# Optimization experiments

Measured on AMD Instinct MI355X. Metric: run time of the kernel, lower is better.

## Reference

```python
import jax, jax.numpy as jnp
import numpy as np

B, N, H, DH, ORDER, DEG = 64, 256, 8, 64, 4, 16
D = H * DH
TOTAL = B * N
E = TOTAL * DEG


def setup_inputs() -> dict:
    key = jax.random.key(0)
    ks = jax.random.split(key, 16)
    output = jax.random.normal(ks[0], (N, B, D), dtype=jnp.float32)
    # attention weights: positive, row-normalized like softmax output
    attn = jax.nn.softmax(jax.random.normal(ks[1], (B, H, N, N), dtype=jnp.float32), axis=-1)
    out_each_head = jax.random.normal(ks[2], (B, N, H, DH), dtype=jnp.float32)
    # random graph edges, endpoints within the same graph (global node ids)
    g = jax.random.randint(ks[3], (E,), 0, B)
    s = g * N + jax.random.randint(ks[4], (E,), 0, N)
    d = g * N + jax.random.randint(ks[5], (E,), 0, N)
    edge_index = jnp.stack([s, d], axis=0).astype(jnp.int64)
    # full graphs, no padding: feature_indices[:,0]=graph id, [:,1]=node pos
    fi = jnp.stack([jnp.repeat(jnp.arange(B), N), jnp.tile(jnp.arange(N), B)], axis=1).astype(jnp.int64)
    batch = fi[:, 0]
    sc = 0.1
    params = dict(
        W_gcn=jax.random.normal(ks[6], (ORDER, ORDER)) * sc,
        b_gcn=jnp.zeros((ORDER,), jnp.float32),
        W_lin=jax.random.normal(ks[7], (ORDER, ORDER)) * sc,
        b_lin=jnp.zeros((ORDER,), jnp.float32),
        W_cheb=jax.random.normal(ks[8], (ORDER, DH, DH)) * sc,
        b_cheb=jnp.zeros((DH,), jnp.float32),
        W_cat=jax.random.normal(ks[9], (2 * D, D)) * sc,
        b_cat=jnp.zeros((D,), jnp.float32),
        gamma=jnp.ones((D,), jnp.float32),
        beta=jnp.zeros((D,), jnp.float32),
    )
    return dict(output=output, attn=attn, out_each_head=out_each_head,
                edge_index=edge_index, feature_indices=fi, batch=batch, **params)


def reference(output, attn, out_each_head, edge_index, feature_indices, batch,
              W_gcn, b_gcn, W_lin, b_lin, W_cheb, b_cheb, W_cat, b_cat, gamma, beta):
    Bn, Hn, Nn, _ = attn.shape
    C = W_gcn.shape[0]
    total = Bn * Nn
    NT = Hn * total

    # ---- get_filter_coefficients: GCN over fully-connected attention graphs ----
    # edge weights are detached in the original (edge_weight.detach())
    A = jax.lax.stop_gradient(attn).transpose(1, 0, 2, 3).reshape(Hn * Bn, Nn, Nn)
    A_hat = A + jnp.eye(Nn, dtype=A.dtype)  # add self loops (weight 1)
    deg = A_hat.sum(axis=1)                 # deg_j = sum_i A_hat[i,j]
    dinv = jnp.where(deg > 0, jax.lax.rsqrt(deg), 0.0)  # (HB, N)
    # x = ones, so x @ W_gcn is a constant row = column sums of W_gcn
    w_row = W_gcn.sum(axis=0)               # (C,)
    s = jnp.einsum('bi,bij->bj', dinv, A_hat) * dinv     # (HB, N)
    x_c = jnp.tanh(s[:, :, None] * w_row + b_gcn)        # (HB, N, C)
    gap = x_c.mean(axis=1)                  # global avg pool per graph (HB, C)
    coeff = gap @ W_lin + b_lin             # (HB, C) rows ordered (head, batch)

    # ---- dynamic Chebyshev filtering per head on the input graph ----
    offsets = (jnp.arange(Hn) * total).astype(edge_index.dtype)
    src = (edge_index[0][None, :] + offsets[:, None]).reshape(-1)
    dst = (edge_index[1][None, :] + offsets[:, None]).reshape(-1)
    deg_n = jax.ops.segment_sum(jnp.ones(src.shape[0], jnp.float32), dst, num_segments=NT)
    dinv_n = jnp.where(deg_n > 0, jax.lax.rsqrt(deg_n), 0.0)
    norm_e = -(dinv_n[src] * dinv_n[dst])   # scaled Laplacian L_hat = -D^-1/2 A D^-1/2

    def prop(x):  # L_hat @ x via gather/scatter
        return jax.ops.segment_sum(norm_e[:, None] * x[src], dst, num_segments=NT)

    # nodes ordered (head, batch, node)
    x0 = out_each_head.transpose(2, 0, 1, 3).reshape(NT, DH)
    batch_all = (batch[None, :] + (jnp.arange(Hn) * Bn)[:, None]).reshape(-1)  # graph id h*B+b
    c_node = coeff[batch_all]               # (NT, ORDER) per-node dynamic coefficients

    T_prev, T_cur = x0, prop(x0)
    acc = c_node[:, 0:1] * (T_prev @ W_cheb[0]) + c_node[:, 1:2] * (T_cur @ W_cheb[1])
    for k in range(2, C):
        T_next = 2.0 * prop(T_cur) - T_prev
        acc = acc + c_node[:, k:k + 1] * (T_next @ W_cheb[k])
        T_prev, T_cur = T_cur, T_next
    acc = acc + b_cheb                      # (NT, DH)

    # regroup heads: (H, B*N, DH) -> (B*N, H*DH), scatter back to (N, B, D)
    filtered = acc.reshape(Hn, total, DH).transpose(1, 0, 2).reshape(total, Hn * DH)
    out_filtered = jnp.zeros_like(output).at[feature_indices[:, 1], feature_indices[:, 0], :].set(filtered)

    # skip connection + linear_cat + final LayerNorm
    out_cat = jnp.concatenate([output, out_filtered], axis=-1)
    out = out_cat @ W_cat + b_cat
    mu = out.mean(axis=-1, keepdims=True)
    var = ((out - mu) ** 2).mean(axis=-1, keepdims=True)
    out = (out - mu) * jax.lax.rsqrt(var + 1e-5) * gamma + beta
    return out
```

## Files before the change

kernel.cpp:

```cpp
#include <hip/hip_runtime.h>
#include <stdint.h>

#define Bq      64
#define Nq      256
#define Hq      8
#define DHq     64
#define TOTALq  16384
#define NTq     131072
#define Dq      512

typedef __attribute__((ext_vector_type(8))) short short8;
typedef __attribute__((ext_vector_type(4))) float floatx4;

__device__ __forceinline__ unsigned short f2bf(float f) {
    union { float f; unsigned int u; } c; c.f = f;
    unsigned int u = c.u;
    return (unsigned short)((u + 0x7fffu + ((u >> 16) & 1u)) >> 16);
}
__device__ __forceinline__ float bf2f(unsigned short u) {
    union { unsigned int u; float f; } c; c.u = ((unsigned int)u) << 16;
    return c.f;
}


__global__ void count_deg_kernel(const int* __restrict__ dstp, int* __restrict__ cnt, int E) {
    int e = blockIdx.x * 256 + threadIdx.x;
    if (e < E) atomicAdd(&cnt[dstp[e]], 1);
}

__global__ void pscatter_kernel(const int* __restrict__ srcp, const int* __restrict__ dstp,
                                const int* __restrict__ cnt, float* __restrict__ Pf, int E) {
    int e = blockIdx.x * 256 + threadIdx.x;
    if (e >= E) return;
    int s = srcp[e], d = dstp[e];
    int cs = cnt[s], cd = cnt[d];
    float dvs = (cs > 0) ? rsqrtf((float)cs) : 0.0f;
    float dvd = (cd > 0) ? rsqrtf((float)cd) : 0.0f;
    int g = d >> 8;
    atomicAdd(&Pf[((size_t)g << 16) + ((size_t)(d & 255) << 8) + (s & 255)],
              -(dvs * dvd));
}

__global__ void pconv_kernel(const float* __restrict__ Pf, unsigned short* __restrict__ Pb) {
    int i = (blockIdx.x * 256 + threadIdx.x) * 4;
    float4 v = *(const float4*)(Pf + i);
    unsigned int lo = (unsigned int)f2bf(v.x) | ((unsigned int)f2bf(v.y) << 16);
    unsigned int hi = (unsigned int)f2bf(v.z) | ((unsigned int)f2bf(v.w) << 16);
    *(uint2*)(Pb + i) = make_uint2(lo, hi);
}

__global__ void prep_kernel(const float* __restrict__ Wcat, unsigned short* __restrict__ Wt2,
                            const float* __restrict__ Wch, float* __restrict__ WchTf) {
    int bid = blockIdx.x;
    if (bid < 256) {
        int idx = bid * 256 + threadIdx.x;
        int col = idx & 511;
        int ktq = idx >> 9;
        const float* src = Wcat + (size_t)(ktq * 8) * 512 + col;
        unsigned int pk[4];
#pragma unroll
        for (int q2 = 0; q2 < 4; ++q2) {
            unsigned short a = f2bf(src[(q2 * 2 + 0) * 512]);
            unsigned short b = f2bf(src[(q2 * 2 + 1) * 512]);
            pk[q2] = (unsigned int)a | ((unsigned int)b << 16);
        }
        *(uint4*)(Wt2 + (size_t)idx * 8) = make_uint4(pk[0], pk[1], pk[2], pk[3]);
    } else {
        int idx = (bid - 256) * 256 + threadIdx.x;
        int k = idx >> 12, rem = idx & 4095;
        int n = rem >> 6, j = rem & 63;
        WchTf[idx] = Wch[(k << 12) + (j << 6) + n];
    }
}

__global__ __launch_bounds__(512)
void coeff_kernel(const float* __restrict__ attn,
                  const float* __restrict__ Wg, const float* __restrict__ bg,
                  const float* __restrict__ Wlin, const float* __restrict__ blin,
                  float* __restrict__ coeff) {
    __shared__ floatx4 part[8][64];
    __shared__ floatx4 dinv4[64];
    const int g = blockIdx.x;
    const int h = g >> 6;
    const int b = g & 63;
    const float* A = attn + ((size_t)(b * Hq + h)) * (Nq * Nq);
    const int tid = threadIdx.x;
    const int rg = tid >> 6;
    const int cv = tid & 63;
    const float* Ap = A + cv * 4;

    floatx4 s1 = (floatx4){0.f, 0.f, 0.f, 0.f};
#pragma unroll 8
    for (int r = 0; r < 32; ++r)
        s1 += *(const floatx4*)(Ap + (size_t)(rg * 32 + r) * 256);
    part[rg][cv] = s1;
    __syncthreads();

    if (tid < 64) {
        floatx4 cs = part[0][tid];
#pragma unroll
        for (int i = 1; i < 8; ++i) cs += part[i][tid];
        floatx4 dv;
#pragma unroll
        for (int i = 0; i < 4; ++i) dv[i] = rsqrtf(cs[i] + 1.0f);
        dinv4[tid] = dv;
    }
    __syncthreads();

    const float* dsc = (const float*)dinv4;
    floatx4 s2 = (floatx4){0.f, 0.f, 0.f, 0.f};
#pragma unroll 8
    for (int r = 0; r < 32; ++r) {
        int rr = rg * 32 + r;
        s2 += dsc[rr] * (*(const floatx4*)(Ap + (size_t)rr * 256));
    }
    part[rg][cv] = s2;
    __syncthreads();

    if (tid < 64) {
        floatx4 ws = part[0][tid];
#pragma unroll
        for (int i = 1; i < 8; ++i) ws += part[i][tid];
        floatx4 dv = dinv4[tid];
        floatx4 sj = (ws + dv) * dv;

        float wr[4], bgl[4];
#pragma unroll
        for (int c = 0; c < 4; ++c) {
            wr[c]  = Wg[0 * 4 + c] + Wg[1 * 4 + c] + Wg[2 * 4 + c] + Wg[3 * 4 + c];
            bgl[c] = bg[c];
        }
        float v[4];
#pragma unroll
        for (int c = 0; c < 4; ++c) {
            v[c] = tanhf(sj[0] * wr[c] + bgl[c]) + tanhf(sj[1] * wr[c] + bgl[c]) +
                   tanhf(sj[2] * wr[c] + bgl[c]) + tanhf(sj[3] * wr[c] + bgl[c]);
#pragma unroll
            for (int o = 32; o >= 1; o >>= 1) v[c] += __shfl_down(v[c], o, 64);
        }
        float g0 = __shfl(v[0], 0, 64), g1 = __shfl(v[1], 0, 64);
        float g2 = __shfl(v[2], 0, 64), g3 = __shfl(v[3], 0, 64);
        if (tid < 4) {
            float r = blin[tid] + (g0 * Wlin[0 * 4 + tid] + g1 * Wlin[1 * 4 + tid] +
                                   g2 * Wlin[2 * 4 + tid] + g3 * Wlin[3 * 4 + tid]) *
                                      (1.0f / 256.0f);
            coeff[g * 4 + tid] = r;
        }
    }
}

__global__ __launch_bounds__(512, 2)
void cheb_fused(const unsigned short* __restrict__ Pb, const float* __restrict__ oeh,
                const float* __restrict__ WchTf, const float* __restrict__ coeff,
                const float* __restrict__ bch, unsigned short* __restrict__ filtb) {
    extern __shared__ unsigned char sm[];
    unsigned short* cm = (unsigned short*)sm;
    unsigned short* rm = (unsigned short*)(sm + 32768);
    unsigned short* Wl = (unsigned short*)(sm + 65536);

    const int g = blockIdx.x;
    const int b = (g & 7) * 8 + ((g >> 3) & 7);
    const int h = g >> 6;
    const int tid = threadIdx.x;
    const int lane = tid & 63, wv = tid >> 6;
    const int wr = wv >> 1, wc = wv & 1;
    const int quad = lane >> 4, l15 = lane & 15;

    const unsigned short* Pbase = Pb + ((size_t)b << 16);
    const float* cf = coeff + (h * 64 + b) * 4;

    {
        const int sn = tid >> 1;
        const int sh = (tid & 1) * 32;
        const float* sp = oeh + (size_t)(b * 256 + sn) * 512 + h * 64 + sh;
        unsigned int pk[16];
#pragma unroll
        for (int j = 0; j < 8; ++j) {
            float4 v = *(const float4*)(sp + j * 4);
            pk[2 * j]     = (unsigned)f2bf(v.x) | ((unsigned)f2bf(v.y) << 16);
            pk[2 * j + 1] = (unsigned)f2bf(v.z) | ((unsigned)f2bf(v.w) << 16);
        }
#pragma unroll
        for (int jj = 0; jj < 4; ++jj)
            *(uint4*)(rm + sn * 64 + ((((sh >> 3) + jj) ^ (sn & 7)) << 3)) =
                make_uint4(pk[4 * jj], pk[4 * jj + 1], pk[4 * jj + 2], pk[4 * jj + 3]);
#pragma unroll
        for (int e = 0; e < 32; ++e) {
            int c = sh + e;
            unsigned short v =
                (unsigned short)((e & 1) ? (pk[e >> 1] >> 16) : (pk[e >> 1] & 0xffffu));
            cm[c * 256 + (((sn >> 3) ^ (c & 31)) << 3) + (sn & 7)] = v;
        }
        float ck = cf[0];
        int r = tid >> 3, su = tid & 7;
        const float* wp = WchTf + r * 64 + su * 8;
        float4 w0 = *(const float4*)wp, w1 = *(const float4*)(wp + 4);
        *(uint4*)(Wl + r * 72 + su * 8) = make_uint4(
            (unsigned)f2bf(w0.x * ck) | ((unsigned)f2bf(w0.y * ck) << 16),
            (unsigned)f2bf(w0.z * ck) | ((unsigned)f2bf(w0.w * ck) << 16),
            (unsigned)f2bf(w1.x * ck) | ((unsigned)f2bf(w1.y * ck) << 16),
            (unsigned)f2bf(w1.z * ck) | ((unsigned)f2bf(w1.w * ck) << 16));
    }
    __syncthreads();

    unsigned int curp[4][2][2], prvp[4][2][2];
#pragma unroll
    for (int rt = 0; rt < 4; ++rt)
#pragma unroll
        for (int ct = 0; ct < 2; ++ct)
#pragma unroll
            for (int p = 0; p < 2; ++p) {
                int m = wr * 64 + rt * 16 + quad * 4 + 2 * p;
                int c = wc * 32 + ct * 16 + l15;
                curp[rt][ct][p] = *(const unsigned int*)(cm + c * 256 +
                                                         (((m >> 3) ^ (c & 31)) << 3) + (m & 7));
                prvp[rt][ct][p] = 0u;
            }

    floatx4 accf[4][2];
#pragma unroll
    for (int rt = 0; rt < 4; ++rt)
#pragma unroll
        for (int ct = 0; ct < 2; ++ct) accf[rt][ct] = (floatx4){0.f, 0.f, 0.f, 0.f};

#pragma unroll
    for (int k = 0; k < 4; ++k) {
#pragma unroll
        for (int kk = 0; kk < 2; ++kk) {
            short8 af[4], bfw[2];
#pragma unroll
            for (int rt = 0; rt < 4; ++rt) {
                int row = wr * 64 + rt * 16 + l15;
                af[rt] = *(const short8*)(rm + row * 64 + (((kk * 4 + quad) ^ (row & 7)) << 3));
            }
#pragma unroll
            for (int ct = 0; ct < 2; ++ct) {
                int oc = wc * 32 + ct * 16 + l15;
                bfw[ct] = *(const short8*)(Wl + oc * 72 + kk * 32 + quad * 8);
            }
#pragma unroll
            for (int rt = 0; rt < 4; ++rt)
#pragma unroll
                for (int ct = 0; ct < 2; ++ct)
                    accf[rt][ct] = __builtin_amdgcn_mfma_f32_16x16x32_bf16(
                        af[rt], bfw[ct], accf[rt][ct], 0, 0, 0);
        }
        if (k < 3) {
            floatx4 accp[4][2];
#pragma unroll
            for (int rt = 0; rt < 4; ++rt)
#pragma unroll
                for (int ct = 0; ct < 2; ++ct) accp[rt][ct] = (floatx4){0.f, 0.f, 0.f, 0.f};
#pragma unroll
            for (int kt = 0; kt < 8; ++kt) {
                short8 ap[4], bp[2];
#pragma unroll
                for (int rt = 0; rt < 4; ++rt) {
                    int row = wr * 64 + rt * 16 + l15;
                    ap[rt] = *(const short8*)(Pbase + row * 256 + kt * 32 + quad * 8);
                }
#pragma unroll
                for (int ct = 0; ct < 2; ++ct) {
                    int c = wc * 32 + ct * 16 + l15;
                    bp[ct] = *(const short8*)(cm + c * 256 + (((kt * 4 + quad) ^ (c & 31)) << 3));
                }
#pragma unroll
                for (int rt = 0; rt < 4; ++rt)
#pragma unroll
                    for (int ct = 0; ct < 2; ++ct)
                        accp[rt][ct] = __builtin_amdgcn_mfma_f32_16x16x32_bf16(
                            ap[rt], bp[ct], accp[rt][ct], 0, 0, 0);
            }
            __syncthreads();
#pragma unroll
            for (int rt = 0; rt < 4; ++rt)
#pragma unroll
                for (int ct = 0; ct < 2; ++ct)
#pragma unroll
                    for (int p = 0; p < 2; ++p) {
                        float a0 = accp[rt][ct][2 * p], a1 = accp[rt][ct][2 * p + 1];
                        if (k > 0) {
                            unsigned pv = prvp[rt][ct][p];
                            a0 = 2.0f * a0 - bf2f((unsigned short)(pv & 0xffffu));
                            a1 = 2.0f * a1 - bf2f((unsigned short)(pv >> 16));
                        }
                        unsigned nv = (unsigned)f2bf(a0) | ((unsigned)f2bf(a1) << 16);
                        prvp[rt][ct][p] = curp[rt][ct][p];
                        curp[rt][ct][p] = nv;
                        int m = wr * 64 + rt * 16 + quad * 4 + 2 * p;
                        int c = wc * 32 + ct * 16 + l15;
                        if (k < 2)
                            *(unsigned int*)(cm + c * 256 + (((m >> 3) ^ (c & 31)) << 3) +
                                             (m & 7)) = nv;
                        rm[m * 64 + (((c >> 3) ^ (m & 7)) << 3) + (c & 7)] =
                            (unsigned short)(nv & 0xffffu);
                        rm[(m + 1) * 64 + (((c >> 3) ^ ((m + 1) & 7)) << 3) + (c & 7)] =
                            (unsigned short)(nv >> 16);
                    }
            {
                float ck = cf[k + 1];
                int r = tid >> 3, su = tid & 7;
                const float* wp = WchTf + (k + 1) * 4096 + r * 64 + su * 8;
                float4 w0 = *(const float4*)wp, w1 = *(const float4*)(wp + 4);
                *(uint4*)(Wl + r * 72 + su * 8) = make_uint4(
                    (unsigned)f2bf(w0.x * ck) | ((unsigned)f2bf(w0.y * ck) << 16),
                    (unsigned)f2bf(w0.z * ck) | ((unsigned)f2bf(w0.w * ck) << 16),
                    (unsigned)f2bf(w1.x * ck) | ((unsigned)f2bf(w1.y * ck) << 16),
                    (unsigned)f2bf(w1.z * ck) | ((unsigned)f2bf(w1.w * ck) << 16));
            }
            __syncthreads();
        }
    }

    float bias[2];
#pragma unroll
    for (int ct = 0; ct < 2; ++ct) bias[ct] = bch[wc * 32 + ct * 16 + l15];
#pragma unroll
    for (int rt = 0; rt < 4; ++rt)
#pragma unroll
        for (int ct = 0; ct < 2; ++ct) {
            int c = wc * 32 + ct * 16 + l15;
#pragma unroll
            for (int i = 0; i < 4; ++i) {
                int m = wr * 64 + rt * 16 + quad * 4 + i;
                filtb[((size_t)m * 64 + b) * 512 + h * 64 + c] =
                    f2bf(accf[rt][ct][i] + bias[ct]);
            }
        }
}

__global__ __launch_bounds__(512, 2)
void gemm_ln_mfma(const float* __restrict__ outp, const unsigned short* __restrict__ filtb,
                  const unsigned short* __restrict__ Wt2, const float* __restrict__ bcat,
                  const float* __restrict__ gamma, const float* __restrict__ beta,
                  float* __restrict__ out) {
    extern __shared__ unsigned char smc[];
    unsigned short* A_lds0 = (unsigned short*)smc;
    unsigned short* A_lds1 = (unsigned short*)(smc + 4096);
    float* ep = (float*)smc;

    const int tid = threadIdx.x;
    const int lane = tid & 63;
    const int wv = tid >> 6;
    const int quad = lane >> 4;
    const int l15 = lane & 15;
    const int r0 = blockIdx.x * 64;

    const int s_row = tid >> 3;
    const int s_sub = tid & 7;
    const int s_q   = s_sub >> 1;
    const int s_e   = (s_sub & 1) * 4;

    const size_t boff = (size_t)(quad * 512 + wv * 64 + l15) * 8;

    floatx4 acc[4][4];
#pragma unroll
    for (int rt = 0; rt < 4; ++rt)
#pragma unroll
        for (int ct = 0; ct < 4; ++ct) acc[rt][ct] = (floatx4){0.f, 0.f, 0.f, 0.f};

    short8 bA[4], bB[4];
    float4 avX_f, avY_f;
    uint2  avX_b, avY_b;

    {
#pragma unroll
        for (int ct = 0; ct < 4; ++ct)
            bA[ct] = *(const short8*)(Wt2 + boff + ct * 128);
#pragma unroll
        for (int ct = 0; ct < 4; ++ct)
            bB[ct] = *(const short8*)(Wt2 + (size_t)16384 + boff + ct * 128);
        float4 av = *(const float4*)(outp + (size_t)(r0 + s_row) * 512 + s_sub * 4);
        avY_f = *(const float4*)(outp + (size_t)(r0 + s_row) * 512 + 32 + s_sub * 4);
        uint2 ap;
        ap.x = (unsigned int)f2bf(av.x) | ((unsigned int)f2bf(av.y) << 16);
        ap.y = (unsigned int)f2bf(av.z) | ((unsigned int)f2bf(av.w) << 16);
        *(uint2*)(A_lds0 + (s_q * 64 + s_row) * 8 + s_e) = ap;
        __syncthreads();
    }

#define GSTEP(KT, BCUR, AC, AN, AVCF, AVCB, AVNF, AVNB)                             \
    do {                                                                            \
        const int kt_ = (KT);                                                       \
        if (kt_ <= 29) {                                                            \
            const int kc2_ = (kt_ + 2) * 32;                                        \
            if (kc2_ < 512)                                                         \
                AVNF = *(const float4*)(outp + (size_t)(r0 + s_row) * 512 +         \
                                        kc2_ + s_sub * 4);                          \
            else                                                                    \
                AVNB = *(const uint2*)(filtb + (size_t)(r0 + s_row) * 512 +         \
                                       (kc2_ - 512) + s_sub * 4);                   \
        }                                                                           \
        short8 af_[4];                                                              \
        _Pragma("unroll")                                                           \
        for (int rt = 0; rt < 4; ++rt)                                              \
            af_[rt] = *(const short8*)(AC + (quad * 64 + rt * 16 + l15) * 8);       \
        _Pragma("unroll")                                                           \
        for (int rt = 0; rt < 4; ++rt)                                              \
            _Pragma("unroll")                                                       \
            for (int ct = 0; ct < 4; ++ct)                                          \
                acc[rt][ct] = __builtin_amdgcn_mfma_f32_16x16x32_bf16(              \
                    af_[rt], BCUR[ct], acc[rt][ct], 0, 0, 0);                       \
        if (kt_ <= 29) {                                                            \
            _Pragma("unroll")                                                       \
            for (int ct = 0; ct < 4; ++ct)                                          \
                BCUR[ct] = *(const short8*)(Wt2 + (size_t)(kt_ + 2) * 16384 +       \
                                            boff + ct * 128);                       \
        }                                                                           \
        if (kt_ <= 30) {                                                            \
            uint2 ap_;                                                              \
            if ((kt_ + 1) * 32 < 512) {                                             \
                ap_.x = (unsigned int)f2bf(AVCF.x) | ((unsigned int)f2bf(AVCF.y) << 16); \
                ap_.y = (unsigned int)f2bf(AVCF.z) | ((unsigned int)f2bf(AVCF.w) << 16); \
            } else {                                                                \
                ap_ = AVCB;                                                         \
            }                                                                       \
            *(uint2*)(AN + (s_q * 64 + s_row) * 8 + s_e) = ap_;                     \
        }                                                                           \
        asm volatile("s_waitcnt lgkmcnt(0)" ::: "memory");                          \
        __builtin_amdgcn_s_barrier();                                               \
        __builtin_amdgcn_sched_barrier(0);                                          \
    } while (0)

    for (int kt2 = 0; kt2 < 16; ++kt2) {
        GSTEP(2 * kt2,     bA, A_lds0, A_lds1, avY_f, avY_b, avX_f, avX_b);
        GSTEP(2 * kt2 + 1, bB, A_lds1, A_lds0, avX_f, avX_b, avY_f, avY_b);
    }
#undef GSTEP

    float gg[8], bb[8];
#pragma unroll
    for (int i = 0; i < 8; ++i) { gg[i] = gamma[i * 64 + lane]; bb[i] = beta[i * 64 + lane]; }
    float bc[4];
#pragma unroll
    for (int ct = 0; ct < 4; ++ct) bc[ct] = bcat[wv * 64 + ct * 16 + l15];

    for (int half = 0; half < 2; ++half) {
        __syncthreads();
#pragma unroll
        for (int rt2 = 0; rt2 < 2; ++rt2) {
            const int rt = half * 2 + rt2;
#pragma unroll
            for (int ct = 0; ct < 4; ++ct) {
                const int col = wv * 64 + ct * 16 + l15;
#pragma unroll
                for (int i = 0; i < 4; ++i) {
                    const int row_l = rt2 * 16 + quad * 4 + i;
                    ep[row_l * 512 + col] = acc[rt][ct][i] + bc[ct];
                }
            }
        }
        __syncthreads();
#pragma unroll
        for (int m4 = 0; m4 < 4; ++m4) {
            const int m = wv * 4 + m4;
            float s = 0.0f, ss = 0.0f;
#pragma unroll
            for (int i = 0; i < 8; ++i) {
                float v = ep[m * 512 + i * 64 + lane];
                s += v; ss += v * v;
            }
#pragma unroll
            for (int o = 32; o >= 1; o >>= 1) {
                s += __shfl_down(s, o, 64);
                ss += __shfl_down(ss, o, 64);
            }
            s = __shfl(s, 0, 64);
            ss = __shfl(ss, 0, 64);
            const float mu = s * (1.0f / 512.0f);
            const float var = ss * (1.0f / 512.0f) - mu * mu;
            const float rs = rsqrtf(var + 1e-5f);
            const int r = r0 + half * 32 + m;
#pragma unroll
            for (int i = 0; i < 8; ++i) {
                const int d = i * 64 + lane;
                out[(size_t)r * 512 + d] = (ep[m * 512 + d] - mu) * rs * gg[i] + bb[i];
            }
        }
    }
}

extern "C" void kernel_launch(void* const* d_in, const int* in_sizes, int n_in,
                              void* d_out, int out_size, void* d_ws, size_t ws_size,
                              hipStream_t stream) {
    const float* output       = (const float*)d_in[0];
    const float* attn         = (const float*)d_in[1];
    const float* oeh          = (const float*)d_in[2];
    const int*   edge_index   = (const int*)d_in[3];
    const float* W_gcn        = (const float*)d_in[6];
    const float* b_gcn        = (const float*)d_in[7];
    const float* W_lin        = (const float*)d_in[8];
    const float* b_lin        = (const float*)d_in[9];
    const float* W_cheb       = (const float*)d_in[10];
    const float* b_cheb       = (const float*)d_in[11];
    const float* W_cat        = (const float*)d_in[12];
    const float* b_cat        = (const float*)d_in[13];
    const float* gamma        = (const float*)d_in[14];
    const float* beta         = (const float*)d_in[15];
    float* out = (float*)d_out;

    const int E = in_sizes[3] / 2;
    const int* srcp = edge_index;
    const int* dstp = edge_index + E;

    uint8_t* ws = (uint8_t*)d_ws;
    size_t cur = 0;
    auto alloc = [&](size_t bytes) -> void* {
        void* p = ws + cur;
        cur += (bytes + 255) & ~(size_t)255;
        return p;
    };
    int*   cnt     = (int*)alloc(TOTALq * sizeof(int));
    float* Pf      = (float*)alloc((size_t)64 * 65536 * sizeof(float));
    unsigned short* Pb   = (unsigned short*)alloc((size_t)64 * 65536 * 2);
    float* coeff   = (float*)alloc(512 * 4 * sizeof(float));
    float* WchTf   = (float*)alloc(4 * 64 * 64 * sizeof(float));
    unsigned short* Wt2  = (unsigned short*)alloc((size_t)Dq * 1024 * 2);
    unsigned short* filtb = (unsigned short*)alloc((size_t)TOTALq * Dq * 2);
    (void)ws_size; (void)n_in; (void)out_size;

    hipMemsetAsync(cnt, 0, TOTALq * sizeof(int), stream);
    count_deg_kernel<<<(E + 255) / 256, 256, 0, stream>>>(dstp, cnt, E);
    hipMemsetAsync(Pf, 0, (size_t)64 * 65536 * sizeof(float), stream);
    pscatter_kernel<<<(E + 255) / 256, 256, 0, stream>>>(srcp, dstp, cnt, Pf, E);
    pconv_kernel<<<4096, 256, 0, stream>>>(Pf, Pb);

    coeff_kernel<<<Hq * Bq, 512, 0, stream>>>(attn, W_gcn, b_gcn, W_lin, b_lin, coeff);
    prep_kernel<<<320, 256, 0, stream>>>(W_cat, Wt2, W_cheb, WchTf);

    cheb_fused<<<512, 512, 74752, stream>>>(Pb, oeh, WchTf, coeff, b_cheb, filtb);

    gemm_ln_mfma<<<TOTALq / 64, 512, 65536, stream>>>(output, filtb, Wt2, b_cat,
                                                      gamma, beta, out);
}
```

Measured before the change: 402.9 us.

## Merge coefficient, degree count, weight prep and Pf zeroing into one front kernel

Combines four independent front-end steps into a single kernel launch with block-range dispatch: the attention-based coefficient computation, the degree-count atomics, the W_cat/W_cheb weight repacking, and zeroing of the dense P buffer (which replaces a memset). The coefficient path now holds its 32 attention rows in registers, so the second pass reuses them instead of reading global memory again. The aim is to cut launch overhead and let these small jobs overlap on the GPU. In exchange, register pressure in the coefficient blocks rises (launch bound 512,1), and the heavy coefficient blocks share a grid with many light ones.

```diff
diff --git a/kernel.cpp b/kernel.cpp
--- a/kernel.cpp
+++ b/kernel.cpp
@@ -20,12 +20,6 @@
 __device__ __forceinline__ float bf2f(unsigned short u) {
     union { unsigned int u; float f; } c; c.u = ((unsigned int)u) << 16;
     return c.f;
-}
-
-
-__global__ void count_deg_kernel(const int* __restrict__ dstp, int* __restrict__ cnt, int E) {
-    int e = blockIdx.x * 256 + threadIdx.x;
-    if (e < E) atomicAdd(&cnt[dstp[e]], 1);
 }
 
 __global__ void pscatter_kernel(const int* __restrict__ srcp, const int* __restrict__ dstp,
@@ -49,103 +43,124 @@
     *(uint2*)(Pb + i) = make_uint2(lo, hi);
 }
 
-__global__ void prep_kernel(const float* __restrict__ Wcat, unsigned short* __restrict__ Wt2,
-                            const float* __restrict__ Wch, float* __restrict__ WchTf) {
-    int bid = blockIdx.x;
-    if (bid < 256) {
-        int idx = bid * 256 + threadIdx.x;
-        int col = idx & 511;
-        int ktq = idx >> 9;
-        const float* src = Wcat + (size_t)(ktq * 8) * 512 + col;
-        unsigned int pk[4];
-#pragma unroll
-        for (int q2 = 0; q2 < 4; ++q2) {
-            unsigned short a = f2bf(src[(q2 * 2 + 0) * 512]);
-            unsigned short b = f2bf(src[(q2 * 2 + 1) * 512]);
-            pk[q2] = (unsigned int)a | ((unsigned int)b << 16);
-        }
-        *(uint4*)(Wt2 + (size_t)idx * 8) = make_uint4(pk[0], pk[1], pk[2], pk[3]);
-    } else {
-        int idx = (bid - 256) * 256 + threadIdx.x;
-        int k = idx >> 12, rem = idx & 4095;
-        int n = rem >> 6, j = rem & 63;
-        WchTf[idx] = Wch[(k << 12) + (j << 6) + n];
-    }
-}
-
-__global__ __launch_bounds__(512)
-void coeff_kernel(const float* __restrict__ attn,
+__global__ __launch_bounds__(512, 1)
+void front_kernel(const float* __restrict__ attn,
                   const float* __restrict__ Wg, const float* __restrict__ bg,
                   const float* __restrict__ Wlin, const float* __restrict__ blin,
-                  float* __restrict__ coeff) {
+                  float* __restrict__ coeff,
+                  const int* __restrict__ dstp, int* __restrict__ cnt, int E,
+                  const float* __restrict__ Wcat, unsigned short* __restrict__ Wt2,
+                  const float* __restrict__ Wch, float* __restrict__ WchTf,
+                  float* __restrict__ Pf) {
     __shared__ floatx4 part[8][64];
     __shared__ floatx4 dinv4[64];
-    const int g = blockIdx.x;
-    const int h = g >> 6;
-    const int b = g & 63;
-    const float* A = attn + ((size_t)(b * Hq + h)) * (Nq * Nq);
+    const int bid = blockIdx.x;
     const int tid = threadIdx.x;
-    const int rg = tid >> 6;
-    const int cv = tid & 63;
-    const float* Ap = A + cv * 4;
-
-    floatx4 s1 = (floatx4){0.f, 0.f, 0.f, 0.f};
-#pragma unroll 8
-    for (int r = 0; r < 32; ++r)
-        s1 += *(const floatx4*)(Ap + (size_t)(rg * 32 + r) * 256);
-    part[rg][cv] = s1;
-    __syncthreads();
-
-    if (tid < 64) {
-        floatx4 cs = part[0][tid];
-#pragma unroll
-        for (int i = 1; i < 8; ++i) cs += part[i][tid];
-        floatx4 dv;
-#pragma unroll
-        for (int i = 0; i < 4; ++i) dv[i] = rsqrtf(cs[i] + 1.0f);
-        dinv4[tid] = dv;
-    }
-    __syncthreads();
-
-    const float* dsc = (const float*)dinv4;
-    floatx4 s2 = (floatx4){0.f, 0.f, 0.f, 0.f};
-#pragma unroll 8
-    for (int r = 0; r < 32; ++r) {
-        int rr = rg * 32 + r;
-        s2 += dsc[rr] * (*(const floatx4*)(Ap + (size_t)rr * 256));
-    }
-    part[rg][cv] = s2;
-    __syncthreads();
-
-    if (tid < 64) {
-        floatx4 ws = part[0][tid];
-#pragma unroll
-        for (int i = 1; i < 8; ++i) ws += part[i][tid];
-        floatx4 dv = dinv4[tid];
-        floatx4 sj = (ws + dv) * dv;
-
-        float wr[4], bgl[4];
-#pragma unroll
-        for (int c = 0; c < 4; ++c) {
-            wr[c]  = Wg[0 * 4 + c] + Wg[1 * 4 + c] + Wg[2 * 4 + c] + Wg[3 * 4 + c];
-            bgl[c] = bg[c];
-        }
-        float v[4];
-#pragma unroll
-        for (int c = 0; c < 4; ++c) {
-            v[c] = tanhf(sj[0] * wr[c] + bgl[c]) + tanhf(sj[1] * wr[c] + bgl[c]) +
-                   tanhf(sj[2] * wr[c] + bgl[c]) + tanhf(sj[3] * wr[c] + bgl[c]);
-#pragma unroll
-            for (int o = 32; o >= 1; o >>= 1) v[c] += __shfl_down(v[c], o, 64);
-        }
-        float g0 = __shfl(v[0], 0, 64), g1 = __shfl(v[1], 0, 64);
-        float g2 = __shfl(v[2], 0, 64), g3 = __shfl(v[3], 0, 64);
-        if (tid < 4) {
-            float r = blin[tid] + (g0 * Wlin[0 * 4 + tid] + g1 * Wlin[1 * 4 + tid] +
-                                   g2 * Wlin[2 * 4 + tid] + g3 * Wlin[3 * 4 + tid]) *
-                                      (1.0f / 256.0f);
-            coeff[g * 4 + tid] = r;
-        }
+
+    if (bid < 512) {
+        const int g = bid;
+        const int h = g >> 6;
+        const int b = g & 63;
+        const float* A = attn + ((size_t)(b * Hq + h)) * (Nq * Nq);
+        const int rg = tid >> 6;
+        const int cv = tid & 63;
+        const float* Ap = A + cv * 4;
+
+        floatx4 regs[32];
+        floatx4 s1 = (floatx4){0.f, 0.f, 0.f, 0.f};
+#pragma unroll
+        for (int r = 0; r < 32; ++r) {
+            regs[r] = *(const floatx4*)(Ap + (size_t)(rg * 32 + r) * 256);
+            s1 += regs[r];
+        }
+        part[rg][cv] = s1;
+        __syncthreads();
+
+        if (tid < 64) {
+            floatx4 cs = part[0][tid];
+#pragma unroll
+            for (int i = 1; i < 8; ++i) cs += part[i][tid];
+            floatx4 dv;
+#pragma unroll
+            for (int i = 0; i < 4; ++i) dv[i] = rsqrtf(cs[i] + 1.0f);
+            dinv4[tid] = dv;
+        }
+        __syncthreads();
+
+        const float* dsc = (const float*)dinv4;
+        floatx4 s2 = (floatx4){0.f, 0.f, 0.f, 0.f};
+#pragma unroll
+        for (int r = 0; r < 32; ++r)
+            s2 += dsc[rg * 32 + r] * regs[r];
+        part[rg][cv] = s2;
+        __syncthreads();
+
+        if (tid < 64) {
+            floatx4 ws = part[0][tid];
+#pragma unroll
+            for (int i = 1; i < 8; ++i) ws += part[i][tid];
+            floatx4 dv = dinv4[tid];
+            floatx4 sj = (ws + dv) * dv;
+
+            float wr[4], bgl[4];
+#pragma unroll
+            for (int c = 0; c < 4; ++c) {
+                wr[c]  = Wg[0 * 4 + c] + Wg[1 * 4 + c] + Wg[2 * 4 + c] + Wg[3 * 4 + c];
+                bgl[c] = bg[c];
+            }
+            float v[4];
+#pragma unroll
+            for (int c = 0; c < 4; ++c) {
+                v[c] = tanhf(sj[0] * wr[c] + bgl[c]) + tanhf(sj[1] * wr[c] + bgl[c]) +
+                       tanhf(sj[2] * wr[c] + bgl[c]) + tanhf(sj[3] * wr[c] + bgl[c]);
+#pragma unroll
+                for (int o = 32; o >= 1; o >>= 1) v[c] += __shfl_down(v[c], o, 64);
+            }
+            float g0 = __shfl(v[0], 0, 64), g1 = __shfl(v[1], 0, 64);
+            float g2 = __shfl(v[2], 0, 64), g3 = __shfl(v[3], 0, 64);
+            if (tid < 4) {
+                float r = blin[tid] + (g0 * Wlin[0 * 4 + tid] + g1 * Wlin[1 * 4 + tid] +
+                                       g2 * Wlin[2 * 4 + tid] + g3 * Wlin[3 * 4 + tid]) *
+                                          (1.0f / 256.0f);
+                coeff[g * 4 + tid] = r;
+            }
+        }
+        return;
+    }
+
+    const int nbCnt = (E + 511) >> 9;
+    if (bid < 512 + nbCnt) {
+        int e = (bid - 512) * 512 + tid;
+        if (e < E) atomicAdd(&cnt[dstp[e]], 1);
+        return;
+    }
+    if (bid < 512 + nbCnt + 160) {
+        int pb = bid - 512 - nbCnt;
+        if (pb < 128) {
+            int idx = pb * 512 + tid;
+            int col = idx & 511;
+            int ktq = idx >> 9;
+            const float* src = Wcat + (size_t)(ktq * 8) * 512 + col;
+            unsigned int pk[4];
+#pragma unroll
+            for (int q2 = 0; q2 < 4; ++q2) {
+                unsigned short a = f2bf(src[(q2 * 2 + 0) * 512]);
+                unsigned short b = f2bf(src[(q2 * 2 + 1) * 512]);
+                pk[q2] = (unsigned int)a | ((unsigned int)b << 16);
+            }
+            *(uint4*)(Wt2 + (size_t)idx * 8) = make_uint4(pk[0], pk[1], pk[2], pk[3]);
+        } else {
+            int idx = (pb - 128) * 512 + tid;
+            int k = idx >> 12, rem = idx & 4095;
+            int n = rem >> 6, j = rem & 63;
+            WchTf[idx] = Wch[(k << 12) + (j << 6) + n];
+        }
+        return;
+    }
+    {
+        int zb = bid - 512 - nbCnt - 160;
+        size_t i = ((size_t)zb * 512 + tid) * 4;
+        *(float4*)(Pf + i) = make_float4(0.f, 0.f, 0.f, 0.f);
     }
 }
 
@@ -520,14 +535,16 @@
     (void)ws_size; (void)n_in; (void)out_size;
 
     hipMemsetAsync(cnt, 0, TOTALq * sizeof(int), stream);
-    count_deg_kernel<<<(E + 255) / 256, 256, 0, stream>>>(dstp, cnt, E);
-    hipMemsetAsync(Pf, 0, (size_t)64 * 65536 * sizeof(float), stream);
+
+    const int nbCnt = (E + 511) / 512;
+    const int frontGrid = 512 + nbCnt + 160 + 2048;
+    front_kernel<<<frontGrid, 512, 0, stream>>>(attn, W_gcn, b_gcn, W_lin, b_lin, coeff,
+                                                dstp, cnt, E, W_cat, Wt2, W_cheb, WchTf,
+                                                Pf);
+
     pscatter_kernel<<<(E + 255) / 256, 256, 0, stream>>>(srcp, dstp, cnt, Pf, E);
     pconv_kernel<<<4096, 256, 0, stream>>>(Pf, Pb);
 
-    coeff_kernel<<<Hq * Bq, 512, 0, stream>>>(attn, W_gcn, b_gcn, W_lin, b_lin, coeff);
-    prep_kernel<<<320, 256, 0, stream>>>(W_cat, Wt2, W_cheb, WchTf);
-
     cheb_fused<<<512, 512, 74752, stream>>>(Pb, oeh, WchTf, coeff, b_cheb, filtb);
 
     gemm_ln_mfma<<<TOTALq / 64, 512, 65536, stream>>>(output, filtb, Wt2, b_cat,
```

Result: faster. 381.4 us (-5.3%).
